# Kernel optimization log

Measured on AMD Instinct MI355X. Metric: run time of the kernel, lower is better.

## Reference

```python
import jax, jax.numpy as jnp
import numpy as np

NU, NT, E, H = 100000, 200000, 1000000, 64
NUM_LAYERS = 3


def setup_inputs() -> dict:
    key = jax.random.key(0)
    ks = jax.random.split(key, 16)
    s = 0.05
    inp = {}
    inp["x_user"] = jax.random.normal(ks[0], (NU, 32), jnp.float32)
    inp["x_transaction"] = jax.random.normal(ks[1], (NT, 64), jnp.float32)
    inp["ei_u2u"] = jax.random.randint(ks[2], (2, E), 0, NU, jnp.int32)
    inp["ei_t2t"] = jax.random.randint(ks[3], (2, E), 0, NT, jnp.int32)
    inp["ei_u2t"] = jnp.stack([jax.random.randint(ks[4], (E,), 0, NU),
                               jax.random.randint(ks[5], (E,), 0, NT)]).astype(jnp.int32)
    inp["ei_t2u"] = jnp.stack([jax.random.randint(ks[6], (E,), 0, NT),
                               jax.random.randint(ks[7], (E,), 0, NU)]).astype(jnp.int32)
    inp["W_emb_user"] = jax.random.normal(ks[8], (32, H), jnp.float32) * s
    inp["b_emb_user"] = jnp.zeros((H,), jnp.float32)
    inp["W_emb_txn"] = jax.random.normal(ks[9], (64, H), jnp.float32) * s
    inp["b_emb_txn"] = jnp.zeros((H,), jnp.float32)
    # one GCNConv weight/bias per (layer, edge_type): order u2u, t2t, u2t, t2u
    inp["conv_W"] = jax.random.normal(ks[10], (NUM_LAYERS, 4, H, H), jnp.float32) * s
    inp["conv_b"] = jnp.zeros((NUM_LAYERS, 4, H), jnp.float32)
    inp["W1"] = jax.random.normal(ks[11], (H, H), jnp.float32) * s
    inp["b1"] = jnp.zeros((H,), jnp.float32)
    inp["W2"] = jax.random.normal(ks[12], (H, 1), jnp.float32) * s
    inp["b2"] = jnp.zeros((1,), jnp.float32)
    return inp


def _gcn(h_src, ei, n_src, n_dst, W, b, self_loops):
    """GCNConv: x W with symmetric degree normalization, scatter-sum into dst."""
    src, dst = ei[0], ei[1]
    if self_loops:  # same node type on both ends: add self loops (PyG default)
        loop = jnp.arange(n_dst, dtype=src.dtype)
        src = jnp.concatenate([src, loop])
        dst = jnp.concatenate([dst, loop])
        deg = jax.ops.segment_sum(jnp.ones_like(dst, jnp.float32), dst, num_segments=n_dst)
        dinv = jnp.where(deg > 0, jax.lax.rsqrt(jnp.maximum(deg, 1.0)), 0.0)
        norm = dinv[src] * dinv[dst]
    else:  # bipartite relation: out-degree of src, in-degree of dst
        ds = jax.ops.segment_sum(jnp.ones_like(src, jnp.float32), src, num_segments=n_src)
        dd = jax.ops.segment_sum(jnp.ones_like(dst, jnp.float32), dst, num_segments=n_dst)
        dsi = jnp.where(ds > 0, jax.lax.rsqrt(jnp.maximum(ds, 1.0)), 0.0)
        ddi = jnp.where(dd > 0, jax.lax.rsqrt(jnp.maximum(dd, 1.0)), 0.0)
        norm = dsi[src] * ddi[dst]
    m = h_src @ W  # [N_src, H] transform first (GCNConv order)
    out = jax.ops.segment_sum(m[src] * norm[:, None], dst, num_segments=n_dst)
    return out + b


def reference(x_user, x_transaction, ei_u2u, ei_t2t, ei_u2t, ei_t2u,
              W_emb_user, b_emb_user, W_emb_txn, b_emb_txn,
              conv_W, conv_b, W1, b1, W2, b2):
    hu = x_user @ W_emb_user + b_emb_user          # [NU, H]
    ht = x_transaction @ W_emb_txn + b_emb_txn     # [NT, H]
    for l in range(NUM_LAYERS):
        ou1 = _gcn(hu, ei_u2u, NU, NU, conv_W[l, 0], conv_b[l, 0], True)
        ot1 = _gcn(ht, ei_t2t, NT, NT, conv_W[l, 1], conv_b[l, 1], True)
        ot2 = _gcn(hu, ei_u2t, NU, NT, conv_W[l, 2], conv_b[l, 2], False)
        ou2 = _gcn(ht, ei_t2u, NT, NU, conv_W[l, 3], conv_b[l, 3], False)
        # HeteroConv aggr='mean' across relations per dst type, then ReLU
        hu = jax.nn.relu((ou1 + ou2) * 0.5)
        ht = jax.nn.relu((ot1 + ot2) * 0.5)
    g = jnp.stack([hu.mean(axis=0), ht.mean(axis=0)])  # [2, H] per-type global mean
    x = g.mean(axis=0, keepdims=True)                  # [1, H]
    x = jax.nn.relu(x @ W1 + b1)                       # dropout is identity at eval
    return jax.nn.sigmoid(x @ W2 + b2)                 # [1, 1]
```

## Files before the change

### kernel.cpp

```cpp
#include <hip/hip_runtime.h>
#include <hip/hip_bf16.h>
#include <hip/hip_fp8.h>

#define NU_ 100000
#define NT_ 200000
#define NE_ 1000000
#define HD  64
#define NL  3

#define OFF0 0
#define OFF1 (NU_)
#define OFF4 (2 * NU_ + 2 * NT_)
#define OFF5 (3 * NU_ + 2 * NT_)
#define HTOT (3 * NU_ + 3 * NT_)
#define RPT2 (NU_ + NT_)

#define PB1  512
#define BKP  2048
#define NBKC 147
#define NBKS 147
#define NBKT (NBKC + NBKS)

#define WPK_EMBU 0
#define WPK_EMBT 2048
#define WPK_CONV 6144
#define WPK_G0U  55296
#define WPK_G0T  59392
#define WPK_TOT  67584
#define PK_ELEMS (WPK_TOT + 256)
#define PKB      ((PK_ELEMS + 255) / 256)

#define GMU 512
#define GMT 1024
#define GBU 3125
#define GBT 6250

typedef float floatx2 __attribute__((ext_vector_type(2)));
typedef _Float16 f16x8 __attribute__((ext_vector_type(8)));
typedef float f32x4 __attribute__((ext_vector_type(4)));
typedef unsigned short u16x8 __attribute__((ext_vector_type(8)));

__device__ __forceinline__ unsigned char enc_fp8(float v) {
    return (unsigned char)__hip_cvt_float_to_fp8(v, __HIP_SATFINITE, __HIP_E4M3);
}

__device__ __forceinline__ float dec1_fp8(unsigned int u) {
    int e = (u >> 3) & 15;
    int m = u & 7;
    int mant = m | (e ? 8 : 0);
    if (u & 0x80) mant = -mant;
    int ex = (e ? e : 1) - 10;
    return (float)mant * __uint_as_float((unsigned int)(ex + 127) << 23);
}

__device__ __forceinline__ void dec4_fp8(unsigned int u, float* f) {
#if __has_builtin(__builtin_amdgcn_cvt_pk_f32_fp8)
    floatx2 lo = __builtin_amdgcn_cvt_pk_f32_fp8((int)u, false);
    floatx2 hi = __builtin_amdgcn_cvt_pk_f32_fp8((int)u, true);
    f[0] = lo.x; f[1] = lo.y; f[2] = hi.x; f[3] = hi.y;
#else
    f[0] = dec1_fp8(u & 0xff);
    f[1] = dec1_fp8((u >> 8) & 0xff);
    f[2] = dec1_fp8((u >> 16) & 0xff);
    f[3] = dec1_fp8((u >> 24) & 0xff);
#endif
}

__global__ void detect_dtype(const unsigned short* __restrict__ x, int* __restrict__ flag, int n) {
    __shared__ int s_big;
    if (threadIdx.x == 0) s_big = 0;
    __syncthreads();
    int big = 0;
    for (int i = threadIdx.x; i < n; i += blockDim.x) {
        float v = __uint_as_float(((unsigned int)x[i]) << 16);
        if (!(fabsf(v) < 1.0e4f)) big = 1;
    }
    if (big) atomicAdd(&s_big, 1);
    __syncthreads();
    if (threadIdx.x == 0) flag[0] = (s_big > 0) ? 0 : 1;
}

struct Ptr10 { const void* p[10]; };

__global__ void cvt_weights(Ptr10 src, float* __restrict__ dst, float* __restrict__ gsum,
                            const int* __restrict__ flag) {
    const int c[11] = {0, 2048, 2112, 6208, 6272, 55424, 56192, 60288, 60352, 60416, 60417};
    int i = blockIdx.x * blockDim.x + threadIdx.x;
    if (i < 64) gsum[i] = 0.f;
    if (i >= 60417) return;
    int r = 0;
#pragma unroll
    for (int k = 1; k < 10; ++k)
        if (i >= c[k]) r = k;
    int e = i - c[r];
    if (flag[0]) {
        unsigned short u = ((const unsigned short*)src.p[r])[e];
        dst[i] = __uint_as_float(((unsigned int)u) << 16);
    } else {
        dst[i] = ((const float*)src.p[r])[e];
    }
}

__device__ __forceinline__ void pack_dev(int gid, const float* __restrict__ wts,
                                         _Float16* __restrict__ wpk,
                                         float* __restrict__ bcomp) {
    if (gid >= PK_ELEMS) return;
    if (gid < WPK_G0U) {
        const float* W;
        int r, KS;
        if (gid < WPK_EMBT) { W = wts; r = gid; KS = 1; }
        else if (gid < WPK_CONV) { W = wts + 2112; r = gid - WPK_EMBT; KS = 2; }
        else {
            int mat = (gid - WPK_CONV) >> 12;
            W = wts + 6272 + mat * 4096;
            r = (gid - WPK_CONV) & 4095;
            KS = 2;
        }
        int j = r & 7;
        int lane = (r >> 3) & 63;
        int f = r >> 9;
        int ct = f / KS;
        int s = f - ct * KS;
        int k = 32 * s + 8 * (lane >> 4) + j;
        int n = 16 * ct + (lane & 15);
        wpk[gid] = (_Float16)W[k * 64 + n];
    } else if (gid < WPK_TOT) {
        const float* We;
        int matc, rr, KS;
        if (gid < WPK_G0T) {
            int r = gid - WPK_G0U;
            matc = (r >> 11) ? 2 : 0;
            rr = r & 2047;
            We = wts;
            KS = 1;
        } else {
            int r = gid - WPK_G0T;
            matc = (r >> 12) ? 3 : 1;
            rr = r & 4095;
            We = wts + 2112;
            KS = 2;
        }
        const float* Wc = wts + 6272 + matc * 4096;
        int j = rr & 7;
        int lane = (rr >> 3) & 63;
        int f = rr >> 9;
        int ct = f / KS;
        int s = f - ct * KS;
        int k = 32 * s + 8 * (lane >> 4) + j;
        int n = 16 * ct + (lane & 15);
        float acc = 0.f;
#pragma unroll
        for (int q = 0; q < 64; ++q)
            acc = fmaf(We[k * 64 + q], Wc[q * 64 + n], acc);
        wpk[gid] = (_Float16)acc;
    } else {
        int q = gid - WPK_TOT;
        int mat = q >> 6;
        int n = q & 63;
        const float* be = (mat == 0 || mat == 2) ? (wts + 2048) : (wts + 6208);
        const float* Wc = wts + 6272 + mat * 4096;
        float acc = 0.f;
#pragma unroll
        for (int k = 0; k < 64; ++k)
            acc = fmaf(be[k], Wc[k * 64 + n], acc);
        bcomp[q] = acc;
    }
}

__device__ __forceinline__ void p1_dev(int bid, const int* __restrict__ eu2u,
                                       const int* __restrict__ et2t,
                                       const int* __restrict__ eu2t,
                                       const int* __restrict__ et2u,
                                       int* __restrict__ gcnt, int* __restrict__ bofs) {
    __shared__ int cnt[NBKT];
    for (int j = threadIdx.x; j < NBKT; j += 256) cnt[j] = 0;
    __syncthreads();
    for (int i = bid * 256 + threadIdx.x; i < 6 * NE_; i += PB1 * 256) {
        int b;
        if (i < 4 * NE_) {
            int m;
            if (i < NE_)          m = eu2u[i + NE_];
            else if (i < 2 * NE_) m = NU_ + et2t[i];
            else if (i < 3 * NE_) m = NU_ + eu2t[i - NE_];
            else                  m = et2u[i - 2 * NE_];
            b = m >> 11;
        } else {
            int m2 = (i < 5 * NE_) ? eu2t[i - 4 * NE_] : (NU_ + et2u[i - 5 * NE_]);
            b = NBKC + (m2 >> 11);
        }
        atomicAdd(&cnt[b], 1);
    }
    __syncthreads();
    for (int j = threadIdx.x; j < NBKT; j += 256) {
        bofs[bid * NBKT + j] = atomicAdd(&gcnt[j], cnt[j]);
    }
}

__global__ __launch_bounds__(256) void fused_p1_pack(
    const int* __restrict__ eu2u, const int* __restrict__ et2t,
    const int* __restrict__ eu2t, const int* __restrict__ et2u,
    int* __restrict__ gcnt, int* __restrict__ bofs,
    const float* __restrict__ wts, _Float16* __restrict__ wpk, float* __restrict__ bcomp) {
    int b = blockIdx.x;
    if (b < PB1) {
        p1_dev(b, eu2u, et2t, eu2t, et2u, gcnt, bofs);
    } else {
        pack_dev((b - PB1) * 256 + threadIdx.x, wts, wpk, bcomp);
    }
}

__global__ __launch_bounds__(256) void p2_scatter(
    const int* __restrict__ eu2u, const int* __restrict__ et2t,
    const int* __restrict__ eu2t, const int* __restrict__ et2u,
    const int* __restrict__ gcnt, int* __restrict__ gbase, const int* __restrict__ bofs,
    unsigned int* __restrict__ part_csr, unsigned int* __restrict__ part_src) {
    __shared__ int gb[NBKT];
    __shared__ int lofs[NBKT];
    const int t = threadIdx.x;
    for (int j = t; j < NBKT; j += 256) { lofs[j] = 0; gb[j] = gcnt[j]; }
    __syncthreads();
    if (t == 0) {
        int s = 0;
        for (int j = 0; j < NBKC; ++j) { int c = gb[j]; gb[j] = s; s += c; }
        s = 0;
        for (int j = NBKC; j < NBKT; ++j) { int c = gb[j]; gb[j] = s; s += c; }
    }
    __syncthreads();
    const int bid = blockIdx.x;
    if (bid == 0)
        for (int j = t; j < NBKT; j += 256) gbase[j] = gb[j];
    for (int i = bid * 256 + t; i < 6 * NE_; i += PB1 * 256) {
        if (i < 4 * NE_) {
            int m; unsigned int src, tag;
            if (i < NE_)          { m = eu2u[i + NE_];        src = (unsigned int)eu2u[i];           tag = 0u; }
            else if (i < 2 * NE_) { m = NU_ + et2t[i];        src = (unsigned int)et2t[i - NE_];     tag = 0u; }
            else if (i < 3 * NE_) { m = NU_ + eu2t[i - NE_];  src = (unsigned int)eu2t[i - 2 * NE_]; tag = 1u; }
            else                  { m = et2u[i - 2 * NE_];    src = (unsigned int)et2u[i - 3 * NE_]; tag = 1u; }
            int b = m >> 11;
            int l = atomicAdd(&lofs[b], 1);
            int pos = gb[b] + bofs[bid * NBKT + b] + l;
            part_csr[pos] = (src << 12) | (tag << 11) | (unsigned int)(m & (BKP - 1));
        } else {
            int m2 = (i < 5 * NE_) ? eu2t[i - 4 * NE_] : (NU_ + et2u[i - 5 * NE_]);
            int b = NBKC + (m2 >> 11);
            int l = atomicAdd(&lofs[b], 1);
            int pos = gb[b] + bofs[bid * NBKT + b] + l;
            part_src[pos] = (unsigned int)m2;
        }
    }
}

__global__ __launch_bounds__(1024) void bucket_build(
    const unsigned int* __restrict__ part_csr, const unsigned int* __restrict__ part_src,
    const int* __restrict__ gcnt, const int* __restrict__ gbase,
    float* __restrict__ dinv, int4* __restrict__ meta,
    int* __restrict__ colU, int* __restrict__ colT) {
    const int b = blockIdx.x;
    const int t = threadIdx.x;
    if (b >= NBKC) {
        __shared__ int cS[BKP];
        const int n = gcnt[b];
        const int base = gbase[b];
        for (int j = t; j < BKP; j += 1024) cS[j] = 0;
        __syncthreads();
        for (int i = t; i < n; i += 1024)
            atomicAdd(&cS[(int)(part_src[base + i] & (BKP - 1))], 1);
        __syncthreads();
        const int m0 = (b - NBKC) << 11;
        for (int j = t; j < BKP; j += 1024) {
            int m2 = m0 + j;
            if (m2 < NU_ + NT_) {
                int o = (m2 < NU_) ? (OFF4 + m2) : (OFF5 + (m2 - NU_));
                int h = cS[j];
                dinv[o] = (h > 0) ? rsqrtf((float)h) : 0.f;
            }
        }
        return;
    }
    __shared__ int cA[BKP];
    __shared__ int cB[BKP];
    __shared__ int lp[BKP];
    __shared__ int s1[1024];
    const int n = gcnt[b];
    const int base = gbase[b];
    for (int j = t; j < BKP; j += 1024) { cA[j] = 0; cB[j] = 0; }
    __syncthreads();
    for (int i = t; i < n; i += 1024) {
        unsigned int it = part_csr[base + i];
        int l = (int)(it & (BKP - 1));
        if (it & 0x800u) atomicAdd(&cB[l], 1);
        else             atomicAdd(&cA[l], 1);
    }
    __syncthreads();
    const int j0 = t << 1, j1 = j0 + 1;
    const int a0 = cA[j0] + cB[j0];
    const int a1 = cA[j1] + cB[j1];
    const int ps = a0 + a1;
    s1[t] = ps;
    __syncthreads();
    for (int off = 1; off < 1024; off <<= 1) {
        int x = (t >= off) ? s1[t - off] : 0;
        __syncthreads();
        s1[t] += x;
        __syncthreads();
    }
    const int excl = s1[t] - ps;
    lp[j0] = excl;
    lp[j1] = excl + a0;
    __syncthreads();
    const int m0 = b << 11;
    const int gb0 = gbase[b];
    for (int j = t; j < BKP; j += 1024) {
        int m = m0 + j;
        if (m < NU_ + NT_) {
            int hA = cA[j], hB = cB[j];
            float dslf = rsqrtf((float)hA + 1.0f);
            int oA = (m < NU_) ? (OFF0 + m) : (OFF1 + (m - NU_));
            dinv[oA] = dslf;
            int4 mt;
            mt.x = gb0 + lp[j] - ((m >= NU_) ? 2 * NE_ : 0);
            mt.y = hA + hB;
            mt.z = __float_as_int(0.5f * dslf);
            mt.w = __float_as_int((hB > 0) ? 0.5f * rsqrtf((float)hB) : 0.f);
            meta[m] = mt;
        }
    }
    __syncthreads();
    for (int j = t; j < BKP; j += 1024) cA[j] = 0;
    __syncthreads();
    for (int i = t; i < n; i += 1024) {
        unsigned int it = part_csr[base + i];
        int mlow = (int)(it & (BKP - 1));
        int ofs = atomicAdd(&cA[mlow], 1);
        int g = gb0 + lp[mlow] + ofs;
        int colv = (int)(((it >> 12) << 6) | ((it & 0x800u) << 20));
        int m = m0 + mlow;
        if (m < NU_) colU[g] = colv;
        else         colT[g - 2 * NE_] = colv;
    }
}

template <int K>
__device__ __forceinline__ void gemm0_dev(int t0, int tstride, int ntiles,
                                          const void* __restrict__ x,
                                          const _Float16* __restrict__ WApk,
                                          const _Float16* __restrict__ WBpk,
                                          const float* __restrict__ bA,
                                          const float* __restrict__ bB,
                                          const float* __restrict__ scA,
                                          const float* __restrict__ scB,
                                          unsigned char* __restrict__ mA,
                                          unsigned char* __restrict__ mB,
                                          const int* __restrict__ flag) {
    constexpr int KS = K / 32;
    const int lane = threadIdx.x & 63;
    const int rq = lane & 15;
    const int oct = lane >> 4;

    f16x8 bf[2][4][KS];
#pragma unroll
    for (int m = 0; m < 2; ++m) {
        const _Float16* P = m ? WBpk : WApk;
#pragma unroll
        for (int ct = 0; ct < 4; ++ct)
#pragma unroll
            for (int s = 0; s < KS; ++s)
                bf[m][ct][s] = *(const f16x8*)(P + (((ct * KS + s) << 9) + (lane << 3)));
    }
    float bvA[4], bvB[4];
#pragma unroll
    for (int ct = 0; ct < 4; ++ct) { bvA[ct] = bA[16 * ct + rq]; bvB[ct] = bB[16 * ct + rq]; }

    const bool isb = flag[0] != 0;

    for (int t = t0; t < ntiles; t += tstride) {
        const int r0 = t << 4;
        f16x8 a[KS];
        if (isb) {
            const unsigned short* xr = (const unsigned short*)x + (size_t)(r0 + rq) * K + 8 * oct;
#pragma unroll
            for (int s = 0; s < KS; ++s) {
                u16x8 uv = *(const u16x8*)(xr + 32 * s);
                f16x8 v;
#pragma unroll
                for (int j = 0; j < 8; ++j)
                    v[j] = (_Float16)__uint_as_float(((unsigned int)uv[j]) << 16);
                a[s] = v;
            }
        } else {
            const float* xr = (const float*)x + (size_t)(r0 + rq) * K + 8 * oct;
#pragma unroll
            for (int s = 0; s < KS; ++s) {
                float4 x0 = *(const float4*)(xr + 32 * s);
                float4 x1 = *(const float4*)(xr + 32 * s + 4);
                f16x8 v;
                v[0] = (_Float16)x0.x; v[1] = (_Float16)x0.y;
                v[2] = (_Float16)x0.z; v[3] = (_Float16)x0.w;
                v[4] = (_Float16)x1.x; v[5] = (_Float16)x1.y;
                v[6] = (_Float16)x1.z; v[7] = (_Float16)x1.w;
                a[s] = v;
            }
        }

        f32x4 acc[2][4];
#pragma unroll
        for (int m = 0; m < 2; ++m)
#pragma unroll
            for (int ct = 0; ct < 4; ++ct) acc[m][ct] = (f32x4){0.f, 0.f, 0.f, 0.f};
#pragma unroll
        for (int m = 0; m < 2; ++m)
#pragma unroll
            for (int ct = 0; ct < 4; ++ct)
#pragma unroll
                for (int s = 0; s < KS; ++s)
                    acc[m][ct] = __builtin_amdgcn_mfma_f32_16x16x32_f16(a[s], bf[m][ct][s],
                                                                       acc[m][ct], 0, 0, 0);

        const int rb = r0 + (oct << 2);
        float sa[4], sb[4];
#pragma unroll
        for (int g = 0; g < 4; ++g) { sa[g] = scA[rb + g]; sb[g] = scB[rb + g]; }
#pragma unroll
        for (int ct = 0; ct < 4; ++ct)
#pragma unroll
            for (int g = 0; g < 4; ++g) {
                mA[(size_t)(rb + g) * HD + 16 * ct + rq] =
                    enc_fp8((acc[0][ct][g] + bvA[ct]) * sa[g]);
                mB[(size_t)(rb + g) * HD + 16 * ct + rq] =
                    enc_fp8((acc[1][ct][g] + bvB[ct]) * sb[g]);
            }
    }
}

__global__ __launch_bounds__(256) void gemm0_both(
    const void* __restrict__ x_user, const void* __restrict__ x_txn,
    const _Float16* __restrict__ wpk, const float* __restrict__ bcomp,
    const float* __restrict__ dinv,
    unsigned char* __restrict__ m_uu, unsigned char* __restrict__ m_ut,
    unsigned char* __restrict__ m_tt, unsigned char* __restrict__ m_tu,
    const int* __restrict__ flag) {
    int b = blockIdx.x;
    int wid = threadIdx.x >> 6;
    if (b < GMU) {
        gemm0_dev<32>(b * 4 + wid, GMU * 4, NU_ / 16, x_user,
                      wpk + WPK_G0U, wpk + WPK_G0U + 2048,
                      bcomp + 0, bcomp + 128,
                      dinv + OFF0, dinv + OFF4, m_uu, m_ut, flag);
    } else {
        gemm0_dev<64>((b - GMU) * 4 + wid, GMT * 4, NT_ / 16, x_txn,
                      wpk + WPK_G0T, wpk + WPK_G0T + 4096,
                      bcomp + 64, bcomp + 192,
                      dinv + OFF1, dinv + OFF5, m_tt, m_tu, flag);
    }
}

__device__ __forceinline__ void gemm_mfma_dev(int t0, int tstride, int ntiles,
                                              const _Float16* __restrict__ h,
                                              const _Float16* __restrict__ WApk,
                                              const _Float16* __restrict__ WBpk,
                                              const float* __restrict__ scA,
                                              const float* __restrict__ scB,
                                              unsigned char* __restrict__ mA,
                                              unsigned char* __restrict__ mB) {
    const int lane = threadIdx.x & 63;
    const int rq = lane & 15;
    const int oct = lane >> 4;

    f16x8 bf[2][4][2];
#pragma unroll
    for (int m = 0; m < 2; ++m) {
        const _Float16* P = m ? WBpk : WApk;
#pragma unroll
        for (int ct = 0; ct < 4; ++ct)
#pragma unroll
            for (int s = 0; s < 2; ++s)
                bf[m][ct][s] = *(const f16x8*)(P + ((((ct << 1) + s) << 9) + (lane << 3)));
    }

    for (int t = t0; t < ntiles; t += tstride) {
        const int r0 = t << 4;
        const _Float16* hr = h + (size_t)(r0 + rq) * HD + 8 * oct;
        f16x8 a0 = *(const f16x8*)(hr);
        f16x8 a1 = *(const f16x8*)(hr + 32);

        f32x4 acc[2][4];
#pragma unroll
        for (int m = 0; m < 2; ++m)
#pragma unroll
            for (int ct = 0; ct < 4; ++ct) acc[m][ct] = (f32x4){0.f, 0.f, 0.f, 0.f};

#pragma unroll
        for (int m = 0; m < 2; ++m)
#pragma unroll
            for (int ct = 0; ct < 4; ++ct) {
                acc[m][ct] = __builtin_amdgcn_mfma_f32_16x16x32_f16(a0, bf[m][ct][0],
                                                                   acc[m][ct], 0, 0, 0);
                acc[m][ct] = __builtin_amdgcn_mfma_f32_16x16x32_f16(a1, bf[m][ct][1],
                                                                   acc[m][ct], 0, 0, 0);
            }

        const int rb = r0 + (oct << 2);
        float sa[4], sb[4];
#pragma unroll
        for (int g = 0; g < 4; ++g) { sa[g] = scA[rb + g]; sb[g] = scB[rb + g]; }
#pragma unroll
        for (int ct = 0; ct < 4; ++ct)
#pragma unroll
            for (int g = 0; g < 4; ++g) {
                mA[(size_t)(rb + g) * HD + 16 * ct + rq] = enc_fp8(acc[0][ct][g] * sa[g]);
                mB[(size_t)(rb + g) * HD + 16 * ct + rq] = enc_fp8(acc[1][ct][g] * sb[g]);
            }
    }
}

__global__ __launch_bounds__(256) void gemm_dual_both(
    const _Float16* __restrict__ hu, const _Float16* __restrict__ ht,
    const _Float16* __restrict__ W0, const _Float16* __restrict__ Wu2t,
    const _Float16* __restrict__ Wt, const _Float16* __restrict__ Wt2u,
    const float* __restrict__ dinv,
    unsigned char* __restrict__ m_uu, unsigned char* __restrict__ m_ut,
    unsigned char* __restrict__ m_tt, unsigned char* __restrict__ m_tu) {
    int b = blockIdx.x;
    int wid = threadIdx.x >> 6;
    if (b < GMU) {
        gemm_mfma_dev(b * 4 + wid, GMU * 4, NU_ / 16, hu, W0, Wu2t,
                      dinv + OFF0, dinv + OFF4, m_uu, m_ut);
    } else {
        gemm_mfma_dev((b - GMU) * 4 + wid, GMT * 4, NT_ / 16, ht, Wt, Wt2u,
                      dinv + OFF1, dinv + OFF5, m_tt, m_tu);
    }
}

__device__ __forceinline__ void gather_dev(int blk, const unsigned char* __restrict__ msg,
                                           unsigned int offB,
                                           const int4* __restrict__ meta,
                                           const int* __restrict__ col,
                                           const float* __restrict__ ba,
                                           const float* __restrict__ bb,
                                           _Float16* __restrict__ out, int N) {
    const int lane = threadIdx.x & 63;
    const int grp = lane >> 3;
    const int sub = lane & 7;
    const int d = (blk << 5) + ((threadIdx.x >> 6) << 3) + grp;
    const bool valid = d < N;

    int4 mt = make_int4(0, 0, 0, 0);
    if (valid) mt = meta[d];
    const int st = mt.x;
    const int cnt = mt.y;
    const float dA = __int_as_float(mt.z);
    const float dB = __int_as_float(mt.w);
    const unsigned char* msgL = msg + (sub << 3);

    floatx2 acc[4];
#pragma unroll
    for (int q = 0; q < 4; ++q) acc[q] = (floatx2){0.f, 0.f};

    auto consume = [&](uint2 u, float s) {
        floatx2 s2; s2.x = s; s2.y = s;
#if __has_builtin(__builtin_amdgcn_cvt_pk_f32_fp8)
        acc[0] += __builtin_amdgcn_cvt_pk_f32_fp8((int)u.x, false) * s2;
        acc[1] += __builtin_amdgcn_cvt_pk_f32_fp8((int)u.x, true) * s2;
        acc[2] += __builtin_amdgcn_cvt_pk_f32_fp8((int)u.y, false) * s2;
        acc[3] += __builtin_amdgcn_cvt_pk_f32_fp8((int)u.y, true) * s2;
#else
        float f[8];
        dec4_fp8(u.x, f);
        dec4_fp8(u.y, f + 4);
        acc[0].x += f[0] * s; acc[0].y += f[1] * s;
        acc[1].x += f[2] * s; acc[1].y += f[3] * s;
        acc[2].x += f[4] * s; acc[2].y += f[5] * s;
        acc[3].x += f[6] * s; acc[3].y += f[7] * s;
#endif
    };

    if (valid) {
        uint2 uself = *(const uint2*)(msgL + ((unsigned int)d << 6));
        consume(uself, dA);
    }

    int cw = (sub < cnt) ? col[st + sub] : 0;
    int done = 0;
    while (done < cnt) {
        int rem = cnt - done;
        if (rem > 8) rem = 8;

        uint2 ub0, ub1, ub2, ub3, ub4, ub5, ub6, ub7;
        float sc0, sc1, sc2, sc3, sc4, sc5, sc6, sc7;

        auto issue = [&](int p, uint2& ub, float& sc) {
            int c = __shfl(cw, (grp << 3) + p);
            unsigned int off = ((unsigned int)c & 0x7fffffffu) + ((c < 0) ? offB : 0u);
            sc = (p < rem) ? ((c < 0) ? dB : dA) : 0.f;
            ub = *(const uint2*)(msgL + off);
        };

        issue(0, ub0, sc0);
        issue(1, ub1, sc1);
        issue(2, ub2, sc2);
        issue(3, ub3, sc3);
        issue(4, ub4, sc4);
        issue(5, ub5, sc5);
        issue(6, ub6, sc6);
        issue(7, ub7, sc7);

        int nd = done + 8;
        int cw2 = (nd + sub < cnt) ? col[st + nd + sub] : 0;

        consume(ub0, sc0);
        consume(ub1, sc1);
        consume(ub2, sc2);
        consume(ub3, sc3);
        consume(ub4, sc4);
        consume(ub5, sc5);
        consume(ub6, sc6);
        consume(ub7, sc7);

        cw = cw2;
        done = nd;
    }

    if (valid) {
        const int col0 = sub << 3;
        float4 a0 = *(const float4*)(ba + col0);
        float4 a1 = *(const float4*)(ba + col0 + 4);
        float4 c0 = *(const float4*)(bb + col0);
        float4 c1 = *(const float4*)(bb + col0 + 4);
        float af[8] = {acc[0].x, acc[0].y, acc[1].x, acc[1].y,
                       acc[2].x, acc[2].y, acc[3].x, acc[3].y};
        float bf[8] = {a0.x + c0.x, a0.y + c0.y, a0.z + c0.z, a0.w + c0.w,
                       a1.x + c1.x, a1.y + c1.y, a1.z + c1.z, a1.w + c1.w};
        f16x8 o;
#pragma unroll
        for (int k = 0; k < 8; ++k)
            o[k] = (_Float16)fmaxf(af[k] + 0.5f * bf[k], 0.f);
        *(f16x8*)(out + ((size_t)d << 6) + col0) = o;
    }
}

__global__ __launch_bounds__(256) void gather_both(
    const unsigned char* __restrict__ msgU, const unsigned char* __restrict__ msgT,
    const int4* __restrict__ meta,
    const int* __restrict__ colU, const int* __restrict__ colT,
    const float* __restrict__ bU0, const float* __restrict__ bU1,
    const float* __restrict__ bT0, const float* __restrict__ bT1,
    _Float16* __restrict__ hu, _Float16* __restrict__ ht) {
    int b = blockIdx.x;
    if (b < GBU) {
        gather_dev(b, msgU, (unsigned int)NU_ * HD, meta, colU, bU0, bU1, hu, NU_);
    } else {
        gather_dev(b - GBU, msgT, (unsigned int)NT_ * HD, meta + NU_, colT, bT0, bT1, ht, NT_);
    }
}

__global__ __launch_bounds__(256) void colmean_both(const _Float16* __restrict__ hu,
                                                    const _Float16* __restrict__ ht,
                                                    float* __restrict__ gsum) {
    const bool isU = blockIdx.x < 512;
    const _Float16* h = isU ? hu : ht;
    const int n = isU ? NU_ : NT_;
    const float scale = isU ? 0.5f / NU_ : 0.5f / NT_;
    const int blk = isU ? blockIdx.x : blockIdx.x - 512;
    const int lane = threadIdx.x & 63;
    const int w = threadIdx.x >> 6;
    float s = 0.f;
    for (int r = blk * 4 + w; r < n; r += 512 * 4)
        s += (float)h[(size_t)r * HD + lane];
    __shared__ float red[256];
    red[threadIdx.x] = s;
    __syncthreads();
    if (threadIdx.x < 64) {
        float t = red[threadIdx.x] + red[64 + threadIdx.x] + red[128 + threadIdx.x] +
                  red[192 + threadIdx.x];
        atomicAdd(&gsum[lane], t * scale);
    }
}

__global__ void head(const float* __restrict__ g, const float* __restrict__ W1,
                     const float* __restrict__ b1, const float* __restrict__ W2,
                     const float* __restrict__ b2, const int* __restrict__ flag,
                     void* __restrict__ out) {
    const int c = threadIdx.x;
    float x = b1[c];
    for (int k = 0; k < HD; ++k) x = fmaf(g[k], W1[k * HD + c], x);
    x = fmaxf(x, 0.f);
    float t = x * W2[c];
    for (int off = 32; off; off >>= 1) t += __shfl_down(t, off);
    if (c == 0) {
        float z = t + b2[0];
        float s = 1.f / (1.f + expf(-z));
        if (flag[0]) *(__hip_bfloat16*)out = __float2bfloat16(s);
        else *(float*)out = s;
    }
}

extern "C" void kernel_launch(void* const* d_in, const int* in_sizes, int n_in,
                              void* d_out, int out_size, void* d_ws, size_t ws_size,
                              hipStream_t stream) {
    const void* x_user = d_in[0];
    const void* x_txn  = d_in[1];
    const int* ei_u2u = (const int*)d_in[2];
    const int* ei_t2t = (const int*)d_in[3];
    const int* ei_u2t = (const int*)d_in[4];
    const int* ei_t2u = (const int*)d_in[5];

    float* ws = (float*)d_ws;
    _Float16* hu = (_Float16*)ws;
    _Float16* ht = hu + (size_t)NU_ * HD;
    float* dinv = (float*)(ht + (size_t)NT_ * HD);
    float* wts = dinv + HTOT;
    float* gsum = wts + 60432;
    float* bcomp = gsum + 64;
    _Float16* wpk = (_Float16*)(bcomp + 256);
    unsigned char* m_uu = (unsigned char*)(wpk + WPK_TOT);
    unsigned char* m_tu = m_uu + (size_t)NU_ * HD;
    unsigned char* m_tt = m_tu + (size_t)NT_ * HD;
    unsigned char* m_ut = m_tt + (size_t)NT_ * HD;
    int* aux  = (int*)(m_ut + (size_t)NU_ * HD);
    int* colU = aux + 2 * NBKT + PB1 * NBKT;
    int* colT = colU + 2 * NE_;
    int4* meta = (int4*)(colT + 2 * NE_);
    int* dflag = (int*)(meta + RPT2);

    int* gcnt  = aux;
    int* gbase = gcnt + NBKT;
    int* bofs  = gbase + NBKT;

    unsigned int* part_csr = (unsigned int*)m_uu;
    unsigned int* part_src = (unsigned int*)hu;

    float* W1f = wts + 56192;
    float* b1f = W1f + 4096;
    float* W2f = b1f + 64;
    float* b2f = W2f + 64;

    hipMemsetAsync(gcnt, 0, (size_t)NBKT * sizeof(int), stream);

    detect_dtype<<<1, 256, 0, stream>>>((const unsigned short*)x_user, dflag, 2048);
    {
        Ptr10 p;
        for (int k = 0; k < 10; ++k) p.p[k] = d_in[6 + k];
        cvt_weights<<<(60417 + 255) / 256, 256, 0, stream>>>(p, wts, gsum, dflag);
    }

    fused_p1_pack<<<PB1 + PKB, 256, 0, stream>>>(ei_u2u, ei_t2t, ei_u2t, ei_t2u,
                                                 gcnt, bofs, wts, wpk, bcomp);

    p2_scatter<<<PB1, 256, 0, stream>>>(ei_u2u, ei_t2t, ei_u2t, ei_t2u,
                                        gcnt, gbase, bofs, part_csr, part_src);

    bucket_build<<<NBKT, 1024, 0, stream>>>(part_csr, part_src, gcnt, gbase,
                                            dinv, meta, colU, colT);

    for (int l = 0; l < NL; ++l) {
        const float* convbf = wts + 55424;
        const float* B0   = convbf + ((size_t)l * 4 + 0) * HD;
        const float* Bt   = convbf + ((size_t)l * 4 + 1) * HD;
        const float* Bu2t = convbf + ((size_t)l * 4 + 2) * HD;
        const float* Bt2u = convbf + ((size_t)l * 4 + 3) * HD;

        if (l == 0) {
            gemm0_both<<<GMU + GMT, 256, 0, stream>>>(x_user, x_txn, wpk, bcomp, dinv,
                                                      m_uu, m_ut, m_tt, m_tu, dflag);
        } else {
            const _Float16* W0   = wpk + WPK_CONV + ((size_t)l * 4 + 0) * 4096;
            const _Float16* Wt   = wpk + WPK_CONV + ((size_t)l * 4 + 1) * 4096;
            const _Float16* Wu2t = wpk + WPK_CONV + ((size_t)l * 4 + 2) * 4096;
            const _Float16* Wt2u = wpk + WPK_CONV + ((size_t)l * 4 + 3) * 4096;
            gemm_dual_both<<<GMU + GMT, 256, 0, stream>>>(hu, ht, W0, Wu2t, Wt, Wt2u, dinv,
                                                          m_uu, m_ut, m_tt, m_tu);
        }

        gather_both<<<GBU + GBT, 256, 0, stream>>>(m_uu, m_tt,
                                                   meta, colU, colT,
                                                   B0, Bt2u, Bt, Bu2t, hu, ht);
    }

    colmean_both<<<1024, 256, 0, stream>>>(hu, ht, gsum);
    head<<<1, 64, 0, stream>>>(gsum, W1f, b1f, W2f, b2f, dflag, d_out);
}
```

Before: 582.5 us.

## Fuse per-layer gather with next layer's MFMA GEMM using double-buffered message arrays

Each gather block now writes its 32 aggregated rows into shared memory and, in the same kernel, two waves run the next layer's dual MFMA GEMM on those rows, producing the fp8 messages directly. This removes the fp16 hidden-state round trip through global memory and one kernel launch per layer. Message buffers are ping-ponged so the gather of one layer does not overwrite the messages it reads. The gcnt memset is also folded into the weight-conversion kernel. The trade-offs are higher per-block register and shared-memory pressure, half the waves idling during the GEMM, and the weight fragments being reloaded by every block.

Result: faster. 552.8 us (-5.1%).

```diff
diff --git a/kernel.cpp b/kernel.cpp
--- a/kernel.cpp
+++ b/kernel.cpp
@@ -83,10 +83,11 @@
 struct Ptr10 { const void* p[10]; };
 
 __global__ void cvt_weights(Ptr10 src, float* __restrict__ dst, float* __restrict__ gsum,
-                            const int* __restrict__ flag) {
+                            int* __restrict__ gcnt, const int* __restrict__ flag) {
     const int c[11] = {0, 2048, 2112, 6208, 6272, 55424, 56192, 60288, 60352, 60416, 60417};
     int i = blockIdx.x * blockDim.x + threadIdx.x;
     if (i < 64) gsum[i] = 0.f;
+    if (i < NBKT) gcnt[i] = 0;
     if (i >= 60417) return;
     int r = 0;
 #pragma unroll
@@ -454,95 +455,17 @@
     }
 }
 
-__device__ __forceinline__ void gemm_mfma_dev(int t0, int tstride, int ntiles,
-                                              const _Float16* __restrict__ h,
-                                              const _Float16* __restrict__ WApk,
-                                              const _Float16* __restrict__ WBpk,
-                                              const float* __restrict__ scA,
-                                              const float* __restrict__ scB,
-                                              unsigned char* __restrict__ mA,
-                                              unsigned char* __restrict__ mB) {
-    const int lane = threadIdx.x & 63;
-    const int rq = lane & 15;
-    const int oct = lane >> 4;
-
-    f16x8 bf[2][4][2];
-#pragma unroll
-    for (int m = 0; m < 2; ++m) {
-        const _Float16* P = m ? WBpk : WApk;
-#pragma unroll
-        for (int ct = 0; ct < 4; ++ct)
-#pragma unroll
-            for (int s = 0; s < 2; ++s)
-                bf[m][ct][s] = *(const f16x8*)(P + ((((ct << 1) + s) << 9) + (lane << 3)));
-    }
-
-    for (int t = t0; t < ntiles; t += tstride) {
-        const int r0 = t << 4;
-        const _Float16* hr = h + (size_t)(r0 + rq) * HD + 8 * oct;
-        f16x8 a0 = *(const f16x8*)(hr);
-        f16x8 a1 = *(const f16x8*)(hr + 32);
-
-        f32x4 acc[2][4];
-#pragma unroll
-        for (int m = 0; m < 2; ++m)
-#pragma unroll
-            for (int ct = 0; ct < 4; ++ct) acc[m][ct] = (f32x4){0.f, 0.f, 0.f, 0.f};
-
-#pragma unroll
-        for (int m = 0; m < 2; ++m)
-#pragma unroll
-            for (int ct = 0; ct < 4; ++ct) {
-                acc[m][ct] = __builtin_amdgcn_mfma_f32_16x16x32_f16(a0, bf[m][ct][0],
-                                                                   acc[m][ct], 0, 0, 0);
-                acc[m][ct] = __builtin_amdgcn_mfma_f32_16x16x32_f16(a1, bf[m][ct][1],
-                                                                   acc[m][ct], 0, 0, 0);
-            }
-
-        const int rb = r0 + (oct << 2);
-        float sa[4], sb[4];
-#pragma unroll
-        for (int g = 0; g < 4; ++g) { sa[g] = scA[rb + g]; sb[g] = scB[rb + g]; }
-#pragma unroll
-        for (int ct = 0; ct < 4; ++ct)
-#pragma unroll
-            for (int g = 0; g < 4; ++g) {
-                mA[(size_t)(rb + g) * HD + 16 * ct + rq] = enc_fp8(acc[0][ct][g] * sa[g]);
-                mB[(size_t)(rb + g) * HD + 16 * ct + rq] = enc_fp8(acc[1][ct][g] * sb[g]);
-            }
-    }
-}
-
-__global__ __launch_bounds__(256) void gemm_dual_both(
-    const _Float16* __restrict__ hu, const _Float16* __restrict__ ht,
-    const _Float16* __restrict__ W0, const _Float16* __restrict__ Wu2t,
-    const _Float16* __restrict__ Wt, const _Float16* __restrict__ Wt2u,
-    const float* __restrict__ dinv,
-    unsigned char* __restrict__ m_uu, unsigned char* __restrict__ m_ut,
-    unsigned char* __restrict__ m_tt, unsigned char* __restrict__ m_tu) {
-    int b = blockIdx.x;
-    int wid = threadIdx.x >> 6;
-    if (b < GMU) {
-        gemm_mfma_dev(b * 4 + wid, GMU * 4, NU_ / 16, hu, W0, Wu2t,
-                      dinv + OFF0, dinv + OFF4, m_uu, m_ut);
-    } else {
-        gemm_mfma_dev((b - GMU) * 4 + wid, GMT * 4, NT_ / 16, ht, Wt, Wt2u,
-                      dinv + OFF1, dinv + OFF5, m_tt, m_tu);
-    }
-}
-
-__device__ __forceinline__ void gather_dev(int blk, const unsigned char* __restrict__ msg,
-                                           unsigned int offB,
-                                           const int4* __restrict__ meta,
-                                           const int* __restrict__ col,
-                                           const float* __restrict__ ba,
-                                           const float* __restrict__ bb,
-                                           _Float16* __restrict__ out, int N) {
+__device__ __forceinline__ void gather_phase(int d, bool valid,
+                                             const unsigned char* __restrict__ msg,
+                                             unsigned int offB,
+                                             const int4* __restrict__ meta,
+                                             const int* __restrict__ col,
+                                             const float* __restrict__ ba,
+                                             const float* __restrict__ bb,
+                                             float* __restrict__ af) {
     const int lane = threadIdx.x & 63;
     const int grp = lane >> 3;
     const int sub = lane & 7;
-    const int d = (blk << 5) + ((threadIdx.x >> 6) << 3) + grp;
-    const bool valid = d < N;
 
     int4 mt = make_int4(0, 0, 0, 0);
     if (valid) mt = meta[d];
@@ -620,22 +543,18 @@
         done = nd;
     }
 
-    if (valid) {
-        const int col0 = sub << 3;
-        float4 a0 = *(const float4*)(ba + col0);
-        float4 a1 = *(const float4*)(ba + col0 + 4);
-        float4 c0 = *(const float4*)(bb + col0);
-        float4 c1 = *(const float4*)(bb + col0 + 4);
-        float af[8] = {acc[0].x, acc[0].y, acc[1].x, acc[1].y,
-                       acc[2].x, acc[2].y, acc[3].x, acc[3].y};
-        float bf[8] = {a0.x + c0.x, a0.y + c0.y, a0.z + c0.z, a0.w + c0.w,
-                       a1.x + c1.x, a1.y + c1.y, a1.z + c1.z, a1.w + c1.w};
-        f16x8 o;
-#pragma unroll
-        for (int k = 0; k < 8; ++k)
-            o[k] = (_Float16)fmaxf(af[k] + 0.5f * bf[k], 0.f);
-        *(f16x8*)(out + ((size_t)d << 6) + col0) = o;
-    }
+    const int col0 = sub << 3;
+    float4 a0 = *(const float4*)(ba + col0);
+    float4 a1 = *(const float4*)(ba + col0 + 4);
+    float4 c0 = *(const float4*)(bb + col0);
+    float4 c1 = *(const float4*)(bb + col0 + 4);
+    float av[8] = {acc[0].x, acc[0].y, acc[1].x, acc[1].y,
+                   acc[2].x, acc[2].y, acc[3].x, acc[3].y};
+    float bv[8] = {a0.x + c0.x, a0.y + c0.y, a0.z + c0.z, a0.w + c0.w,
+                   a1.x + c1.x, a1.y + c1.y, a1.z + c1.z, a1.w + c1.w};
+#pragma unroll
+    for (int k = 0; k < 8; ++k)
+        af[k] = fmaxf(av[k] + 0.5f * bv[k], 0.f);
 }
 
 __global__ __launch_bounds__(256) void gather_both(
@@ -646,10 +565,113 @@
     const float* __restrict__ bT0, const float* __restrict__ bT1,
     _Float16* __restrict__ hu, _Float16* __restrict__ ht) {
     int b = blockIdx.x;
-    if (b < GBU) {
-        gather_dev(b, msgU, (unsigned int)NU_ * HD, meta, colU, bU0, bU1, hu, NU_);
-    } else {
-        gather_dev(b - GBU, msgT, (unsigned int)NT_ * HD, meta + NU_, colT, bT0, bT1, ht, NT_);
+    const bool isU = b < GBU;
+    const int blk = isU ? b : b - GBU;
+    const int grp = (threadIdx.x & 63) >> 3;
+    const int sub = threadIdx.x & 7;
+    const int d = (blk << 5) + ((threadIdx.x >> 6) << 3) + grp;
+    const int N = isU ? NU_ : NT_;
+    float af[8];
+    gather_phase(d, d < N,
+                 isU ? msgU : msgT, (unsigned int)(isU ? NU_ : NT_) * HD,
+                 isU ? meta : meta + NU_, isU ? colU : colT,
+                 isU ? bU0 : bT0, isU ? bU1 : bT1, af);
+    if (d < N) {
+        _Float16* out = isU ? hu : ht;
+        f16x8 o;
+#pragma unroll
+        for (int k = 0; k < 8; ++k) o[k] = (_Float16)af[k];
+        *(f16x8*)(out + ((size_t)d << 6) + (sub << 3)) = o;
+    }
+}
+
+__global__ __launch_bounds__(256) void gather_gemm_both(
+    const unsigned char* __restrict__ msgU, const unsigned char* __restrict__ msgT,
+    const int4* __restrict__ meta,
+    const int* __restrict__ colU, const int* __restrict__ colT,
+    const float* __restrict__ bU0, const float* __restrict__ bU1,
+    const float* __restrict__ bT0, const float* __restrict__ bT1,
+    const _Float16* __restrict__ WUa, const _Float16* __restrict__ WUb,
+    const _Float16* __restrict__ WTa, const _Float16* __restrict__ WTb,
+    const float* __restrict__ dinv,
+    unsigned char* __restrict__ o_uu, unsigned char* __restrict__ o_ut,
+    unsigned char* __restrict__ o_tt, unsigned char* __restrict__ o_tu) {
+    __shared__ _Float16 hs[32][64];
+    int b = blockIdx.x;
+    const bool isU = b < GBU;
+    const int blk = isU ? b : b - GBU;
+    const int lane = threadIdx.x & 63;
+    const int grp = lane >> 3;
+    const int sub = lane & 7;
+    const int w = threadIdx.x >> 6;
+    const int d = (blk << 5) + (w << 3) + grp;
+    const int N = isU ? NU_ : NT_;
+
+    float af[8];
+    gather_phase(d, d < N,
+                 isU ? msgU : msgT, (unsigned int)(isU ? NU_ : NT_) * HD,
+                 isU ? meta : meta + NU_, isU ? colU : colT,
+                 isU ? bU0 : bT0, isU ? bU1 : bT1, af);
+
+    {
+        const int ld = threadIdx.x >> 3;
+        f16x8 o;
+#pragma unroll
+        for (int k = 0; k < 8; ++k) o[k] = (_Float16)af[k];
+        *(f16x8*)(&hs[ld][sub << 3]) = o;
+    }
+    __syncthreads();
+
+    if (w < 2) {
+        const _Float16* Pa = isU ? WUa : WTa;
+        const _Float16* Pb = isU ? WUb : WTb;
+        unsigned char* mA = isU ? o_uu : o_tt;
+        unsigned char* mB = isU ? o_ut : o_tu;
+        const float* scA = dinv + (isU ? OFF0 : OFF1);
+        const float* scB = dinv + (isU ? OFF4 : OFF5);
+        const int rq = lane & 15;
+        const int oct = lane >> 4;
+
+        f16x8 bf[2][4][2];
+#pragma unroll
+        for (int m = 0; m < 2; ++m) {
+            const _Float16* P = m ? Pb : Pa;
+#pragma unroll
+            for (int ct = 0; ct < 4; ++ct)
+#pragma unroll
+                for (int s = 0; s < 2; ++s)
+                    bf[m][ct][s] = *(const f16x8*)(P + ((((ct << 1) + s) << 9) + (lane << 3)));
+        }
+
+        f16x8 a0 = *(const f16x8*)(&hs[16 * w + rq][8 * oct]);
+        f16x8 a1 = *(const f16x8*)(&hs[16 * w + rq][32 + 8 * oct]);
+
+        f32x4 acc[2][4];
+#pragma unroll
+        for (int m = 0; m < 2; ++m)
+#pragma unroll
+            for (int ct = 0; ct < 4; ++ct) acc[m][ct] = (f32x4){0.f, 0.f, 0.f, 0.f};
+#pragma unroll
+        for (int m = 0; m < 2; ++m)
+#pragma unroll
+            for (int ct = 0; ct < 4; ++ct) {
+                acc[m][ct] = __builtin_amdgcn_mfma_f32_16x16x32_f16(a0, bf[m][ct][0],
+                                                                   acc[m][ct], 0, 0, 0);
+                acc[m][ct] = __builtin_amdgcn_mfma_f32_16x16x32_f16(a1, bf[m][ct][1],
+                                                                   acc[m][ct], 0, 0, 0);
+            }
+
+        const int rb = (blk << 5) + 16 * w + (oct << 2);
+        float sa[4], sb[4];
+#pragma unroll
+        for (int g = 0; g < 4; ++g) { sa[g] = scA[rb + g]; sb[g] = scB[rb + g]; }
+#pragma unroll
+        for (int ct = 0; ct < 4; ++ct)
+#pragma unroll
+            for (int g = 0; g < 4; ++g) {
+                mA[(size_t)(rb + g) * HD + 16 * ct + rq] = enc_fp8(acc[0][ct][g] * sa[g]);
+                mB[(size_t)(rb + g) * HD + 16 * ct + rq] = enc_fp8(acc[1][ct][g] * sb[g]);
+            }
     }
 }
 
@@ -712,11 +734,9 @@
     float* gsum = wts + 60432;
     float* bcomp = gsum + 64;
     _Float16* wpk = (_Float16*)(bcomp + 256);
-    unsigned char* m_uu = (unsigned char*)(wpk + WPK_TOT);
-    unsigned char* m_tu = m_uu + (size_t)NU_ * HD;
-    unsigned char* m_tt = m_tu + (size_t)NT_ * HD;
-    unsigned char* m_ut = m_tt + (size_t)NT_ * HD;
-    int* aux  = (int*)(m_ut + (size_t)NU_ * HD);
+    unsigned char* msg0 = (unsigned char*)(wpk + WPK_TOT);
+    unsigned char* msg1 = msg0 + (size_t)(2 * NU_ + 2 * NT_) * HD;
+    int* aux  = (int*)(msg1 + (size_t)(2 * NU_ + 2 * NT_) * HD);
     int* colU = aux + 2 * NBKT + PB1 * NBKT;
     int* colT = colU + 2 * NE_;
     int4* meta = (int4*)(colT + 2 * NE_);
@@ -726,21 +746,25 @@
     int* gbase = gcnt + NBKT;
     int* bofs  = gbase + NBKT;
 
-    unsigned int* part_csr = (unsigned int*)m_uu;
+    auto uu = [](unsigned char* s) { return s; };
+    auto tu = [](unsigned char* s) { return s + (size_t)NU_ * HD; };
+    auto tt = [](unsigned char* s) { return s + (size_t)(NU_ + NT_) * HD; };
+    auto ut = [](unsigned char* s) { return s + (size_t)(NU_ + 2 * NT_) * HD; };
+
+    unsigned int* part_csr = (unsigned int*)msg1;
     unsigned int* part_src = (unsigned int*)hu;
 
     float* W1f = wts + 56192;
     float* b1f = W1f + 4096;
     float* W2f = b1f + 64;
     float* b2f = W2f + 64;
-
-    hipMemsetAsync(gcnt, 0, (size_t)NBKT * sizeof(int), stream);
+    const float* convbf = wts + 55424;
 
     detect_dtype<<<1, 256, 0, stream>>>((const unsigned short*)x_user, dflag, 2048);
     {
         Ptr10 p;
         for (int k = 0; k < 10; ++k) p.p[k] = d_in[6 + k];
-        cvt_weights<<<(60417 + 255) / 256, 256, 0, stream>>>(p, wts, gsum, dflag);
+        cvt_weights<<<(60417 + 255) / 256, 256, 0, stream>>>(p, wts, gsum, gcnt, dflag);
     }
 
     fused_p1_pack<<<PB1 + PKB, 256, 0, stream>>>(ei_u2u, ei_t2t, ei_u2t, ei_t2u,
@@ -752,26 +776,34 @@
     bucket_build<<<NBKT, 1024, 0, stream>>>(part_csr, part_src, gcnt, gbase,
                                             dinv, meta, colU, colT);
 
-    for (int l = 0; l < NL; ++l) {
-        const float* convbf = wts + 55424;
+    gemm0_both<<<GMU + GMT, 256, 0, stream>>>(x_user, x_txn, wpk, bcomp, dinv,
+                                              uu(msg0), ut(msg0), tt(msg0), tu(msg0), dflag);
+
+    for (int l = 0; l < 2; ++l) {
+        unsigned char* in  = (l == 0) ? msg0 : msg1;
+        unsigned char* out = (l == 0) ? msg1 : msg0;
         const float* B0   = convbf + ((size_t)l * 4 + 0) * HD;
         const float* Bt   = convbf + ((size_t)l * 4 + 1) * HD;
         const float* Bu2t = convbf + ((size_t)l * 4 + 2) * HD;
         const float* Bt2u = convbf + ((size_t)l * 4 + 3) * HD;
-
-        if (l == 0) {
-            gemm0_both<<<GMU + GMT, 256, 0, stream>>>(x_user, x_txn, wpk, bcomp, dinv,
-                                                      m_uu, m_ut, m_tt, m_tu, dflag);
-        } else {
-            const _Float16* W0   = wpk + WPK_CONV + ((size_t)l * 4 + 0) * 4096;
-            const _Float16* Wt   = wpk + WPK_CONV + ((size_t)l * 4 + 1) * 4096;
-            const _Float16* Wu2t = wpk + WPK_CONV + ((size_t)l * 4 + 2) * 4096;
-            const _Float16* Wt2u = wpk + WPK_CONV + ((size_t)l * 4 + 3) * 4096;
-            gemm_dual_both<<<GMU + GMT, 256, 0, stream>>>(hu, ht, W0, Wu2t, Wt, Wt2u, dinv,
-                                                          m_uu, m_ut, m_tt, m_tu);
-        }
-
-        gather_both<<<GBU + GBT, 256, 0, stream>>>(m_uu, m_tt,
+        const _Float16* W0n   = wpk + WPK_CONV + ((size_t)(l + 1) * 4 + 0) * 4096;
+        const _Float16* Wtn   = wpk + WPK_CONV + ((size_t)(l + 1) * 4 + 1) * 4096;
+        const _Float16* Wu2tn = wpk + WPK_CONV + ((size_t)(l + 1) * 4 + 2) * 4096;
+        const _Float16* Wt2un = wpk + WPK_CONV + ((size_t)(l + 1) * 4 + 3) * 4096;
+
+        gather_gemm_both<<<GBU + GBT, 256, 0, stream>>>(
+            uu(in), tt(in), meta, colU, colT,
+            B0, Bt2u, Bt, Bu2t,
+            W0n, Wu2tn, Wtn, Wt2un, dinv,
+            uu(out), ut(out), tt(out), tu(out));
+    }
+
+    {
+        const float* B0   = convbf + (2 * 4 + 0) * HD;
+        const float* Bt   = convbf + (2 * 4 + 1) * HD;
+        const float* Bu2t = convbf + (2 * 4 + 2) * HD;
+        const float* Bt2u = convbf + (2 * 4 + 3) * HD;
+        gather_both<<<GBU + GBT, 256, 0, stream>>>(uu(msg0), tt(msg0),
                                                    meta, colU, colT,
                                                    B0, Bt2u, Bt, Bu2t, hu, ht);
     }
```
